# Performance work log

Measured on AMD Instinct MI355X. Metric: run time of the kernel, lower is better.

## Reference

```python
import jax, jax.numpy as jnp
import numpy as np

EMBED_DIM = 768
NUM_HEADS = 12
HEAD_DIM = EMBED_DIM // NUM_HEADS
SCALE = HEAD_DIM ** -0.5


def setup_inputs() -> dict:
    key = jax.random.key(0)
    ks = jax.random.split(key, 5)
    B, N, D = 2, 4096, EMBED_DIM
    std = 1.0 / np.sqrt(D)
    x = jax.random.normal(ks[0], (B, N, D), dtype=jnp.float32)
    W_qkv = jax.random.normal(ks[1], (D, 3 * D), dtype=jnp.float32) * std
    b_qkv = jax.random.normal(ks[2], (3 * D,), dtype=jnp.float32) * 0.01
    W_proj = jax.random.normal(ks[3], (D, D), dtype=jnp.float32) * std
    b_proj = jax.random.normal(ks[4], (D,), dtype=jnp.float32) * 0.01
    return {"x": x, "W_qkv": W_qkv, "b_qkv": b_qkv, "W_proj": W_proj, "b_proj": b_proj}


def reference(x, W_qkv, b_qkv, W_proj, b_proj):
    B, N, D = x.shape
    H, Hd = NUM_HEADS, HEAD_DIM
    qkv = x @ W_qkv + b_qkv                      # [B, N, 3D]
    qkv = qkv.reshape(B, N, 3, H, Hd)
    qkv = jnp.transpose(qkv, (2, 0, 3, 1, 4))    # [3, B, H, N, Hd]
    q, k, v = qkv[0], qkv[1], qkv[2]
    attn = jnp.einsum('bhqd,bhkd->bhqk', q, k) * SCALE   # [B, H, N, N]
    attn = jax.nn.softmax(attn, axis=-1)
    out = jnp.einsum('bhqk,bhkd->bhqd', attn, v)          # [B, H, N, Hd]
    out = jnp.transpose(out, (0, 2, 1, 3)).reshape(B, N, D)
    return out @ W_proj + b_proj
```

## Files before the change

### kernel.cpp

```cpp
#include <hip/hip_runtime.h>
#include <hip/hip_bf16.h>

typedef __attribute__((ext_vector_type(4))) float f32x4;
typedef __attribute__((ext_vector_type(16))) float f32x16;
typedef __attribute__((ext_vector_type(8))) short s16x8;
typedef __attribute__((ext_vector_type(4))) unsigned int u32x4;

#define MFMA16(a, b, c) __builtin_amdgcn_mfma_f32_16x16x32_bf16(a, b, c, 0, 0, 0)
#define MFMA32(a, b, c) __builtin_amdgcn_mfma_f32_32x32x16_bf16(a, b, c, 0, 0, 0)

__device__ __forceinline__ short f2bf(float f) {
  unsigned u = __builtin_bit_cast(unsigned, f);
  u += 0x7fffu + ((u >> 16) & 1u);
  return (short)(u >> 16);
}
__device__ __forceinline__ float bf2f(unsigned short u) {
  return __builtin_bit_cast(float, ((unsigned)u) << 16);
}
__device__ __forceinline__ unsigned cvtpk(float lo, float hi) {
  unsigned r;
  asm("v_cvt_pk_bf16_f32 %0, %1, %2" : "=v"(r) : "v"(lo), "v"(hi));
  return r;
}
__device__ __forceinline__ float ex2(float x) {
  float r;
  asm("v_exp_f32 %0, %1" : "=v"(r) : "v"(x));
  return r;
}
__device__ __forceinline__ void gl_lds16(const unsigned short* g, short* l) {
  __builtin_amdgcn_global_load_lds(
      (const __attribute__((address_space(1))) unsigned int*)g,
      (__attribute__((address_space(3))) unsigned int*)l, 16, 0, 0);
}

__global__ __launch_bounds__(256) void convert_x(
    const float* __restrict__ X, unsigned short* __restrict__ Xb) {
  const size_t i = ((size_t)blockIdx.x * 256 + threadIdx.x) * 8;
  f32x4 a = *(const f32x4*)(X + i);
  f32x4 b = *(const f32x4*)(X + i + 4);
  s16x8 o;
#pragma unroll
  for (int e = 0; e < 4; ++e) o[e] = f2bf(a[e]);
#pragma unroll
  for (int e = 0; e < 4; ++e) o[4 + e] = f2bf(b[e]);
  *(s16x8*)(Xb + i) = o;
}

__global__ __launch_bounds__(256) void tconv(
    const float* __restrict__ W, unsigned short* __restrict__ Wt,
    int K, int N) {
  __shared__ float T[64][65];
  const int k0 = blockIdx.x * 64, n0 = blockIdx.y * 64;
  const int t = threadIdx.x;
  const int tr = t >> 4, tc = (t & 15) * 4;
#pragma unroll
  for (int i = 0; i < 4; ++i) {
    f32x4 v = *(const f32x4*)&W[(size_t)(k0 + tr + i * 16) * N + n0 + tc];
#pragma unroll
    for (int e = 0; e < 4; ++e) T[tc + e][tr + i * 16] = v[e];
  }
  __syncthreads();
  const int nn = t >> 2, kk = (t & 3) * 16;
  s16x8 o0, o1;
#pragma unroll
  for (int j = 0; j < 8; ++j) o0[j] = f2bf(T[nn][kk + j]);
#pragma unroll
  for (int j = 0; j < 8; ++j) o1[j] = f2bf(T[nn][kk + 8 + j]);
  *(s16x8*)&Wt[(size_t)(n0 + nn) * K + k0 + kk] = o0;
  *(s16x8*)&Wt[(size_t)(n0 + nn) * K + k0 + kk + 8] = o1;
}

__global__ __launch_bounds__(256) void qkv_gemm(
    const unsigned short* __restrict__ Xb, const unsigned short* __restrict__ Wt,
    const float* __restrict__ bias, unsigned short* __restrict__ Qo,
    unsigned short* __restrict__ Ko, unsigned short* __restrict__ VTo) {
  __shared__ __align__(16) short As[128 * 32];
  __shared__ __align__(16) short Bs[128 * 32];
  const int m0 = blockIdx.x * 128, n0 = blockIdx.y * 128;
  const int tid = threadIdx.x, lane = tid & 63, wid = tid >> 6;
  const int wr = wid >> 1, wc = wid & 1;
  const int lr = lane & 15, s4 = lane >> 4;

  const int crow = lane >> 2;
  const int ccol = (lane & 3) ^ (crow & 3);
  const unsigned short* ga0 = Xb + (size_t)(m0 + wid * 32 + crow) * 768 + ccol * 8;
  const unsigned short* ga1 = ga0 + (size_t)16 * 768;
  const unsigned short* gb0 = Wt + (size_t)(n0 + wid * 32 + crow) * 768 + ccol * 8;
  const unsigned short* gb1 = gb0 + (size_t)16 * 768;
  short* lA0 = &As[(wid * 2) * 512];
  short* lA1 = &As[(wid * 2 + 1) * 512];
  short* lB0 = &Bs[(wid * 2) * 512];
  short* lB1 = &Bs[(wid * 2 + 1) * 512];

  f32x4 acc[4][4];
#pragma unroll
  for (int i = 0; i < 4; ++i)
#pragma unroll
    for (int j = 0; j < 4; ++j)
#pragma unroll
      for (int e = 0; e < 4; ++e) acc[i][j][e] = 0.f;

  for (int k0 = 0; k0 < 768; k0 += 32) {
    gl_lds16(ga0 + k0, lA0);
    gl_lds16(ga1 + k0, lA1);
    gl_lds16(gb0 + k0, lB0);
    gl_lds16(gb1 + k0, lB1);
    __syncthreads();
    s16x8 af[4], bfr[4];
#pragma unroll
    for (int mi = 0; mi < 4; ++mi) {
      const int row = wr * 64 + mi * 16 + lr;
      af[mi] = *(const s16x8*)&As[row * 32 + ((s4 ^ (row & 3)) << 3)];
    }
#pragma unroll
    for (int ni = 0; ni < 4; ++ni) {
      const int row = wc * 64 + ni * 16 + lr;
      bfr[ni] = *(const s16x8*)&Bs[row * 32 + ((s4 ^ (row & 3)) << 3)];
    }
#pragma unroll
    for (int mi = 0; mi < 4; ++mi)
#pragma unroll
      for (int ni = 0; ni < 4; ++ni)
        acc[mi][ni] = MFMA16(af[mi], bfr[ni], acc[mi][ni]);
    __syncthreads();
  }

  const float QSC = 0.18033688011f;
  const int lg = lane >> 4;
  const int plg = ((lg & 1) << 1) | ((lg >> 1) & 1);
  const int rbase = m0 + wr * 64 + lg * 4;
#pragma unroll
  for (int ni = 0; ni < 4; ++ni) {
    const int cb = n0 + wc * 64 + ni * 16;
    const int which = cb / 768;
    const int rem = cb - which * 768;
    const int h = rem >> 6;
    const int d = (rem & 63) + lr;
    const float bi = bias[cb + lr];
#pragma unroll
    for (int mi = 0; mi < 4; ++mi) {
#pragma unroll
      for (int j = 0; j < 4; ++j) {
        const int row = rbase + mi * 16 + j;
        const int bb = row >> 12, t = row & 4095;
        const float v = acc[mi][ni][j] + bi;
        const size_t hb = (size_t)(bb * 12 + h);
        if (which == 0)
          Qo[(hb * 4096 + t) * 64 + d] = (unsigned short)f2bf(v * QSC);
        else if (which == 1)
          Ko[(hb * 4096 + t) * 64 + d] = (unsigned short)f2bf(v);
        else {
          const int tp = (t & ~15) + plg * 4 + j;
          VTo[(hb * 64 + d) * 4096 + tp] = (unsigned short)f2bf(v);
        }
      }
    }
  }
}

#define TKV 32

__global__ __launch_bounds__(256) void attn_fwd(
    const unsigned short* __restrict__ Qg, const unsigned short* __restrict__ Kg,
    const unsigned short* __restrict__ VTg,
    unsigned short* __restrict__ Opart, float* __restrict__ Lpart) {
  __shared__ __align__(16) short smem[16384];
  const int lin = blockIdx.x;
  const int wg = (lin & 7) * 96 + (lin >> 3);
  const int qt = wg & 15, bh = (wg >> 4) % 24, sz = wg / 384;
  const int tok0 = sz * TKV * 64;
  const unsigned short* Qh = Qg + (size_t)bh * 4096 * 64;
  const unsigned short* Kh = Kg + (size_t)bh * 4096 * 64;
  const unsigned short* Vh = VTg + (size_t)bh * 4096 * 64;
  const int tid = threadIdx.x, lane = tid & 63, wid = tid >> 6;
  const int l31 = lane & 31, hi = lane >> 5;
  const int sw0 = (l31 + (l31 >> 3)) & 7;
  const int sw1 = (sw0 + 4) & 7;
  const int qbase = qt * 256 + wid * 64;

  s16x8 qfA[4], qfB[4];
#pragma unroll
  for (int db = 0; db < 4; ++db) {
    qfA[db] = *(const s16x8*)&Qh[(size_t)(qbase + l31) * 64 + db * 16 + hi * 8];
    qfB[db] = *(const s16x8*)&Qh[(size_t)(qbase + 32 + l31) * 64 + db * 16 + hi * 8];
  }

  f32x16 zf;
#pragma unroll
  for (int r = 0; r < 16; ++r) zf[r] = 0.f;
  f32x16 oA0 = zf, oA1 = zf, oB0 = zf, oB1 = zf;
  float lsumA = 0.f, lsumB = 0.f;

  const int r0 = wid * 16 + (lane >> 3);
  const int r1 = r0 + 8;
  const int c16 = lane & 7;
  const int sc0 = (c16 ^ ((r0 + (r0 >> 3)) & 7)) << 3;
  const int sc1 = (c16 ^ ((r1 + (r1 >> 3)) & 7)) << 3;
  const unsigned short* kg0 = Kh + (size_t)(tok0 + r0) * 64 + sc0;
  const unsigned short* kg1 = Kh + (size_t)(tok0 + r1) * 64 + sc1;
  const unsigned short* vg0 = Vh + (size_t)r0 * 4096 + tok0 + sc0;
  const unsigned short* vg1 = Vh + (size_t)r1 * 4096 + tok0 + sc1;
  short* const ldsK0 = &smem[(wid * 2) * 512];
  short* const ldsK1 = &smem[(wid * 2 + 1) * 512];
  short* const ldsV0 = &smem[8192 + (wid * 2) * 512];
  short* const ldsV1 = &smem[8192 + (wid * 2 + 1) * 512];

  gl_lds16(kg0, ldsK0);
  gl_lds16(kg1, ldsK1);
  gl_lds16(vg0, ldsV0);
  gl_lds16(vg1, ldsV1);
  __syncthreads();

#define PACK_PF(pfv, sv, bse)                                           \
  {                                                                     \
    u32x4 fw;                                                           \
    fw[0] = cvtpk(sv[bse + 0], sv[bse + 1]);                            \
    fw[1] = cvtpk(sv[bse + 2], sv[bse + 3]);                            \
    fw[2] = cvtpk(sv[bse + 4], sv[bse + 5]);                            \
    fw[3] = cvtpk(sv[bse + 6], sv[bse + 7]);                            \
    pfv = __builtin_bit_cast(s16x8, fw);                                \
  }
#define LSUM_TREE(lsum, sv)                                             \
  {                                                                     \
    float ta[8];                                                        \
    _Pragma("unroll") for (int r = 0; r < 8; ++r) ta[r] = sv[r] + sv[r + 8]; \
    _Pragma("unroll") for (int off = 4; off; off >>= 1)                 \
      _Pragma("unroll") for (int r = 0; r < off; ++r) ta[r] += ta[r + off]; \
    lsum += ta[0];                                                      \
  }

  int cur = 0;
  for (int t = 0; t < TKV; ++t) {
    if (t < TKV - 1) {
      const int nb = (cur ^ 1) * 4096;
      gl_lds16(kg0 + (size_t)(t + 1) * 4096, ldsK0 + nb);
      gl_lds16(kg1 + (size_t)(t + 1) * 4096, ldsK1 + nb);
      gl_lds16(vg0 + (t + 1) * 64, ldsV0 + nb);
      gl_lds16(vg1 + (t + 1) * 64, ldsV1 + nb);
    }
    const short* Kc = smem + cur * 4096;
    const short* Vc = smem + 8192 + cur * 4096;

    {
      f32x16 sA = zf, sB = zf;
      __builtin_amdgcn_s_setprio(1);
#pragma unroll
      for (int db = 0; db < 4; ++db) {
        s16x8 kf = *(const s16x8*)&Kc[l31 * 64 + (((db * 2 + hi) ^ sw0) << 3)];
        sA = MFMA32(kf, qfA[db], sA);
        sB = MFMA32(kf, qfB[db], sB);
      }
      __builtin_amdgcn_s_setprio(0);
#pragma unroll
      for (int r = 0; r < 16; ++r) {
        sA[r] = ex2(sA[r]);
        sB[r] = ex2(sB[r]);
      }
      s16x8 pfA0, pfA1, pfB0, pfB1;
      PACK_PF(pfA0, sA, 0)
      PACK_PF(pfA1, sA, 8)
      PACK_PF(pfB0, sB, 0)
      PACK_PF(pfB1, sB, 8)
      LSUM_TREE(lsumA, sA)
      LSUM_TREE(lsumB, sB)
      __builtin_amdgcn_s_setprio(1);
      s16x8 v0 = *(const s16x8*)&Vc[l31 * 64 + (((0 + hi) ^ sw0) << 3)];
      s16x8 v1 = *(const s16x8*)&Vc[l31 * 64 + (((2 + hi) ^ sw0) << 3)];
      s16x8 w0 = *(const s16x8*)&Vc[(32 + l31) * 64 + (((0 + hi) ^ sw1) << 3)];
      s16x8 w1 = *(const s16x8*)&Vc[(32 + l31) * 64 + (((2 + hi) ^ sw1) << 3)];
      oA0 = MFMA32(v0, pfA0, oA0);
      oA0 = MFMA32(v1, pfA1, oA0);
      oA1 = MFMA32(w0, pfA0, oA1);
      oA1 = MFMA32(w1, pfA1, oA1);
      oB0 = MFMA32(v0, pfB0, oB0);
      oB0 = MFMA32(v1, pfB1, oB0);
      oB1 = MFMA32(w0, pfB0, oB1);
      oB1 = MFMA32(w1, pfB1, oB1);
      __builtin_amdgcn_s_setprio(0);
    }

    {
      f32x16 sA = zf, sB = zf;
      __builtin_amdgcn_s_setprio(1);
#pragma unroll
      for (int db = 0; db < 4; ++db) {
        s16x8 kf = *(const s16x8*)&Kc[(32 + l31) * 64 + (((db * 2 + hi) ^ sw1) << 3)];
        sA = MFMA32(kf, qfA[db], sA);
        sB = MFMA32(kf, qfB[db], sB);
      }
      __builtin_amdgcn_s_setprio(0);
#pragma unroll
      for (int r = 0; r < 16; ++r) {
        sA[r] = ex2(sA[r]);
        sB[r] = ex2(sB[r]);
      }
      s16x8 pfA2, pfA3, pfB2, pfB3;
      PACK_PF(pfA2, sA, 0)
      PACK_PF(pfA3, sA, 8)
      PACK_PF(pfB2, sB, 0)
      PACK_PF(pfB3, sB, 8)
      LSUM_TREE(lsumA, sA)
      LSUM_TREE(lsumB, sB)
      __builtin_amdgcn_s_setprio(1);
      s16x8 v2 = *(const s16x8*)&Vc[l31 * 64 + (((4 + hi) ^ sw0) << 3)];
      s16x8 v3 = *(const s16x8*)&Vc[l31 * 64 + (((6 + hi) ^ sw0) << 3)];
      s16x8 w2 = *(const s16x8*)&Vc[(32 + l31) * 64 + (((4 + hi) ^ sw1) << 3)];
      s16x8 w3 = *(const s16x8*)&Vc[(32 + l31) * 64 + (((6 + hi) ^ sw1) << 3)];
      oA0 = MFMA32(v2, pfA2, oA0);
      oA0 = MFMA32(v3, pfA3, oA0);
      oA1 = MFMA32(w2, pfA2, oA1);
      oA1 = MFMA32(w3, pfA3, oA1);
      oB0 = MFMA32(v2, pfB2, oB0);
      oB0 = MFMA32(v3, pfB3, oB0);
      oB1 = MFMA32(w2, pfB2, oB1);
      oB1 = MFMA32(w3, pfB3, oB1);
      __builtin_amdgcn_s_setprio(0);
    }

    if (t < TKV - 1) {
      __syncthreads();
      cur ^= 1;
    }
  }
#undef LSUM_TREE
#undef PACK_PF

  const float lfullA = lsumA + __shfl_xor(lsumA, 32);
  const float lfullB = lsumB + __shfl_xor(lsumB, 32);
  const int qA = qbase + l31, qB = qbase + 32 + l31;
  const size_t ob = ((size_t)(sz * 24 + bh)) * 64 * 4096;
#pragma unroll
  for (int r = 0; r < 16; ++r) {
    const int dd = (r & 3) + 8 * (r >> 2) + 4 * hi;
    Opart[ob + (size_t)dd * 4096 + qA] = (unsigned short)f2bf(oA0[r]);
    Opart[ob + (size_t)(dd + 32) * 4096 + qA] = (unsigned short)f2bf(oA1[r]);
    Opart[ob + (size_t)dd * 4096 + qB] = (unsigned short)f2bf(oB0[r]);
    Opart[ob + (size_t)(dd + 32) * 4096 + qB] = (unsigned short)f2bf(oB1[r]);
  }
  Lpart[(size_t)(sz * 24 + bh) * 4096 + qA] = lfullA;
  Lpart[(size_t)(sz * 24 + bh) * 4096 + qB] = lfullB;
}

__global__ __launch_bounds__(256) void attn_combine(
    const unsigned short* __restrict__ Opart, const float* __restrict__ Lpart,
    unsigned short* __restrict__ Aout) {
  __shared__ float T[64][65];
  const int q0 = blockIdx.x * 64, bh = blockIdx.y;
  const int t = threadIdx.x;
  const int d = t >> 2, qc = (t & 3) * 16;
  const size_t b0 = ((size_t)bh * 64 + d) * 4096 + q0 + qc;
  const size_t b1 = ((size_t)(24 + bh) * 64 + d) * 4096 + q0 + qc;
  s16x8 a0 = *(const s16x8*)&Opart[b0];
  s16x8 a1 = *(const s16x8*)&Opart[b0 + 8];
  s16x8 c0 = *(const s16x8*)&Opart[b1];
  s16x8 c1 = *(const s16x8*)&Opart[b1 + 8];
#pragma unroll
  for (int e = 0; e < 8; ++e) {
    T[qc + e][d] = bf2f((unsigned short)a0[e]) + bf2f((unsigned short)c0[e]);
    T[qc + 8 + e][d] = bf2f((unsigned short)a1[e]) + bf2f((unsigned short)c1[e]);
  }
  __syncthreads();
  const int q = t >> 2, dc = (t & 3) * 16;
  const float l = Lpart[(size_t)bh * 4096 + q0 + q] +
                  Lpart[(size_t)(24 + bh) * 4096 + q0 + q];
  const float inv = 1.0f / l;
  const int b = bh / 12, h = bh - b * 12;
  s16x8 o0, o1;
#pragma unroll
  for (int e = 0; e < 8; ++e) o0[e] = f2bf(T[q][dc + e] * inv);
#pragma unroll
  for (int e = 0; e < 8; ++e) o1[e] = f2bf(T[q][dc + 8 + e] * inv);
  const size_t gb = ((size_t)(b * 4096 + q0 + q)) * 768 + h * 64 + dc;
  *(s16x8*)&Aout[gb] = o0;
  *(s16x8*)&Aout[gb + 8] = o1;
}

__global__ __launch_bounds__(256) void proj_gemm(
    const unsigned short* __restrict__ A, const unsigned short* __restrict__ Wt,
    const float* __restrict__ bias, float* __restrict__ out) {
  __shared__ __align__(16) short As[128 * 32];
  __shared__ __align__(16) short Bs[128 * 32];
  const int m0 = blockIdx.x * 128, n0 = blockIdx.y * 128;
  const int tid = threadIdx.x, lane = tid & 63, wid = tid >> 6;
  const int wr = wid >> 1, wc = wid & 1;
  const int lr = lane & 15, s4 = lane >> 4;

  const int crow = lane >> 2;
  const int ccol = (lane & 3) ^ (crow & 3);
  const unsigned short* ga0 = A + (size_t)(m0 + wid * 32 + crow) * 768 + ccol * 8;
  const unsigned short* ga1 = ga0 + (size_t)16 * 768;
  const unsigned short* gb0 = Wt + (size_t)(n0 + wid * 32 + crow) * 768 + ccol * 8;
  const unsigned short* gb1 = gb0 + (size_t)16 * 768;
  short* lA0 = &As[(wid * 2) * 512];
  short* lA1 = &As[(wid * 2 + 1) * 512];
  short* lB0 = &Bs[(wid * 2) * 512];
  short* lB1 = &Bs[(wid * 2 + 1) * 512];

  f32x4 acc[4][4];
#pragma unroll
  for (int i = 0; i < 4; ++i)
#pragma unroll
    for (int j = 0; j < 4; ++j)
#pragma unroll
      for (int e = 0; e < 4; ++e) acc[i][j][e] = 0.f;

  for (int k0 = 0; k0 < 768; k0 += 32) {
    gl_lds16(ga0 + k0, lA0);
    gl_lds16(ga1 + k0, lA1);
    gl_lds16(gb0 + k0, lB0);
    gl_lds16(gb1 + k0, lB1);
    __syncthreads();
    s16x8 af[4], bfr[4];
#pragma unroll
    for (int mi = 0; mi < 4; ++mi) {
      const int row = wr * 64 + mi * 16 + lr;
      af[mi] = *(const s16x8*)&As[row * 32 + ((s4 ^ (row & 3)) << 3)];
    }
#pragma unroll
    for (int ni = 0; ni < 4; ++ni) {
      const int row = wc * 64 + ni * 16 + lr;
      bfr[ni] = *(const s16x8*)&Bs[row * 32 + ((s4 ^ (row & 3)) << 3)];
    }
#pragma unroll
    for (int mi = 0; mi < 4; ++mi)
#pragma unroll
      for (int ni = 0; ni < 4; ++ni)
        acc[mi][ni] = MFMA16(af[mi], bfr[ni], acc[mi][ni]);
    __syncthreads();
  }

  const int rbase = m0 + wr * 64 + (lane >> 4) * 4;
#pragma unroll
  for (int ni = 0; ni < 4; ++ni) {
    const int cb = n0 + wc * 64 + ni * 16;
    const float bi = bias[cb + lr];
#pragma unroll
    for (int mi = 0; mi < 4; ++mi) {
#pragma unroll
      for (int j = 0; j < 4; ++j) {
        const int row = rbase + mi * 16 + j;
        out[(size_t)row * 768 + cb + lr] = acc[mi][ni][j] + bi;
      }
    }
  }
}

extern "C" void kernel_launch(void* const* d_in, const int* in_sizes, int n_in,
                              void* d_out, int out_size, void* d_ws, size_t ws_size,
                              hipStream_t stream) {
  const float* x = (const float*)d_in[0];
  const float* W_qkv = (const float*)d_in[1];
  const float* b_qkv = (const float*)d_in[2];
  const float* W_proj = (const float*)d_in[3];
  const float* b_proj = (const float*)d_in[4];
  float* out = (float*)d_out;

  unsigned short* ws = (unsigned short*)d_ws;
  const size_t NQ = (size_t)24 * 4096 * 64;
  unsigned short* q = ws;
  unsigned short* k = ws + NQ;
  unsigned short* vt = ws + 2 * NQ;
  unsigned short* xb_attn = ws + 3 * NQ;
  unsigned short* wqt = ws + 4 * NQ;
  unsigned short* wpt = wqt + (size_t)2304 * 768;

  const size_t base_bytes = (4 * NQ + (size_t)2304 * 768 + (size_t)768 * 768) * 2;
  const size_t opart_bytes = (size_t)2 * 24 * 64 * 4096 * 2;
  unsigned short* Opart = (unsigned short*)((char*)d_ws + base_bytes);
  float* Lpart = (float*)((char*)d_ws + base_bytes + opart_bytes);

  convert_x<<<3072, 256, 0, stream>>>(x, xb_attn);
  tconv<<<dim3(12, 36), 256, 0, stream>>>(W_qkv, wqt, 768, 2304);
  tconv<<<dim3(12, 12), 256, 0, stream>>>(W_proj, wpt, 768, 768);
  qkv_gemm<<<dim3(64, 18), 256, 0, stream>>>(xb_attn, wqt, b_qkv, q, k, vt);
  attn_fwd<<<768, 256, 0, stream>>>(q, k, vt, Opart, Lpart);
  attn_combine<<<dim3(64, 24), 256, 0, stream>>>(Opart, Lpart, xb_attn);
  proj_gemm<<<dim3(64, 6), 256, 0, stream>>>(xb_attn, wpt, b_proj, out);
}
```

Measured before the change: 226.7 us.

## Triple-buffer K/V tiles in LDS with two-ahead prefetch and partial waitcnt

Expands the attention kernel's LDS staging from double to triple buffering, so K/V tiles are prefetched two iterations ahead. The full __syncthreads is replaced by s_waitcnt vmcnt(4) plus a raw barrier, so only the older tile's loads must land before the next iteration. This aims to hide global-to-LDS latency better, at the cost of 1.5x LDS per block, which may reduce occupancy.

```diff
diff --git a/kernel.cpp b/kernel.cpp
--- a/kernel.cpp
+++ b/kernel.cpp
@@ -164,7 +164,7 @@
     const unsigned short* __restrict__ Qg, const unsigned short* __restrict__ Kg,
     const unsigned short* __restrict__ VTg,
     unsigned short* __restrict__ Opart, float* __restrict__ Lpart) {
-  __shared__ __align__(16) short smem[16384];
+  __shared__ __align__(16) short smem[24576];
   const int lin = blockIdx.x;
   const int wg = (lin & 7) * 96 + (lin >> 3);
   const int qt = wg & 15, bh = (wg >> 4) % 24, sz = wg / 384;
@@ -200,16 +200,19 @@
   const unsigned short* kg1 = Kh + (size_t)(tok0 + r1) * 64 + sc1;
   const unsigned short* vg0 = Vh + (size_t)r0 * 4096 + tok0 + sc0;
   const unsigned short* vg1 = Vh + (size_t)r1 * 4096 + tok0 + sc1;
-  short* const ldsK0 = &smem[(wid * 2) * 512];
-  short* const ldsK1 = &smem[(wid * 2 + 1) * 512];
-  short* const ldsV0 = &smem[8192 + (wid * 2) * 512];
-  short* const ldsV1 = &smem[8192 + (wid * 2 + 1) * 512];
-
-  gl_lds16(kg0, ldsK0);
-  gl_lds16(kg1, ldsK1);
-  gl_lds16(vg0, ldsV0);
-  gl_lds16(vg1, ldsV1);
-  __syncthreads();
+  const int wofs0 = (wid * 2) * 512, wofs1 = (wid * 2 + 1) * 512;
+
+  gl_lds16(kg0, &smem[wofs0]);
+  gl_lds16(kg1, &smem[wofs1]);
+  gl_lds16(vg0, &smem[12288 + wofs0]);
+  gl_lds16(vg1, &smem[12288 + wofs1]);
+  gl_lds16(kg0 + 4096, &smem[4096 + wofs0]);
+  gl_lds16(kg1 + 4096, &smem[4096 + wofs1]);
+  gl_lds16(vg0 + 64, &smem[12288 + 4096 + wofs0]);
+  gl_lds16(vg1 + 64, &smem[12288 + 4096 + wofs1]);
+  asm volatile("s_waitcnt vmcnt(4)" ::: "memory");
+  __builtin_amdgcn_s_barrier();
+  __builtin_amdgcn_sched_barrier(0);
 
 #define PACK_PF(pfv, sv, bse)                                           \
   {                                                                     \
@@ -229,17 +232,16 @@
     lsum += ta[0];                                                      \
   }
 
-  int cur = 0;
+  int oc = 0, on = 4096, of = 8192;
   for (int t = 0; t < TKV; ++t) {
-    if (t < TKV - 1) {
-      const int nb = (cur ^ 1) * 4096;
-      gl_lds16(kg0 + (size_t)(t + 1) * 4096, ldsK0 + nb);
-      gl_lds16(kg1 + (size_t)(t + 1) * 4096, ldsK1 + nb);
-      gl_lds16(vg0 + (t + 1) * 64, ldsV0 + nb);
-      gl_lds16(vg1 + (t + 1) * 64, ldsV1 + nb);
-    }
-    const short* Kc = smem + cur * 4096;
-    const short* Vc = smem + 8192 + cur * 4096;
+    if (t + 2 < TKV) {
+      gl_lds16(kg0 + (size_t)(t + 2) * 4096, &smem[of + wofs0]);
+      gl_lds16(kg1 + (size_t)(t + 2) * 4096, &smem[of + wofs1]);
+      gl_lds16(vg0 + (t + 2) * 64, &smem[12288 + of + wofs0]);
+      gl_lds16(vg1 + (t + 2) * 64, &smem[12288 + of + wofs1]);
+    }
+    const short* Kc = smem + oc;
+    const short* Vc = smem + 12288 + oc;
 
     {
       f32x16 sA = zf, sB = zf;
@@ -318,8 +320,17 @@
     }
 
     if (t < TKV - 1) {
-      __syncthreads();
-      cur ^= 1;
+      if (t + 2 < TKV) {
+        asm volatile("s_waitcnt vmcnt(4)" ::: "memory");
+      } else {
+        asm volatile("s_waitcnt vmcnt(0)" ::: "memory");
+      }
+      __builtin_amdgcn_s_barrier();
+      __builtin_amdgcn_sched_barrier(0);
+      const int tmp = oc;
+      oc = on;
+      on = of;
+      of = tmp;
     }
   }
 #undef LSUM_TREE
```

New measurement: 227.0 us. No clear change (+0.1%).
